# Performance work log

Hardware: AMD Instinct MI355X
Metric: run time of the kernel (lower is better)

The kernel has to match this reference:

```python
import jax, jax.numpy as jnp
import numpy as np

N_F = 256
D = 4 * N_F          # d_model after PixelUnshuffle(2)
D_INNER = 2 * D      # mamba expand=2
D_STATE = 16
DT_RANK = D // 16
N_LAYERS = 8
BATCH = 16
IMG = 32


def _pixel_unshuffle(x, r):
    b, c, h, w = x.shape
    x = x.reshape(b, c, h // r, r, w // r, r)
    return x.transpose(0, 1, 3, 5, 2, 4).reshape(b, c * r * r, h // r, w // r)


def _pixel_shuffle(x, r):
    b, c, h, w = x.shape
    co = c // (r * r)
    x = x.reshape(b, co, r, r, h, w)
    return x.transpose(0, 1, 4, 2, 5, 3).reshape(b, co, h * r, w * r)


def _layernorm(x, w, b):
    mu = jnp.mean(x, -1, keepdims=True)
    var = jnp.mean((x - mu) ** 2, -1, keepdims=True)
    return (x - mu) * jax.lax.rsqrt(var + 1e-5) * w + b


def _transpose_xy(a):
    b, l, c = a.shape
    s = int(np.sqrt(l))
    return a.reshape(b, s, s, c).transpose(0, 2, 1, 3).reshape(b, l, c)


def _mamba_mixer(u, W_in_i, conv_w_i, conv_b_i, W_x_i, W_dt_i, b_dt_i, A_log_i, D_skip_i, W_out_i):
    b, l, d = u.shape
    xz = jnp.einsum('bld,ed->ble', u, W_in_i)          # (B,L,2*d_inner)
    x, z = jnp.split(xz, 2, axis=-1)
    # causal depthwise conv over sequence, kernel 4, left-pad 3
    xt = jax.lax.conv_general_dilated(
        x.transpose(0, 2, 1), conv_w_i[:, None, :], (1,), [(3, 0)],
        feature_group_count=D_INNER, dimension_numbers=('NCH', 'OIH', 'NCH'))
    x = jax.nn.silu((xt + conv_b_i[None, :, None]).transpose(0, 2, 1))  # (B,L,d_inner)
    dbc = jnp.einsum('ble,fe->blf', x, W_x_i)          # (B,L,dt_rank+2*d_state)
    dt = jax.nn.softplus(jnp.einsum('blr,er->ble', dbc[..., :DT_RANK], W_dt_i) + b_dt_i)
    Bm = dbc[..., DT_RANK:DT_RANK + D_STATE]
    Cm = dbc[..., DT_RANK + D_STATE:]
    A = -jnp.exp(A_log_i)                              # (d_inner, d_state)

    def step(h, inp):
        dt_t, B_t, C_t, x_t = inp                      # (B,di),(B,ds),(B,ds),(B,di)
        h = jnp.exp(dt_t[..., None] * A) * h + (dt_t * x_t)[..., None] * B_t[:, None, :]
        return h, jnp.einsum('bds,bs->bd', h, C_t)

    h0 = jnp.zeros((b, D_INNER, D_STATE), dtype=u.dtype)
    _, ys = jax.lax.scan(step, h0, (dt.transpose(1, 0, 2), Bm.transpose(1, 0, 2),
                                    Cm.transpose(1, 0, 2), x.transpose(1, 0, 2)))
    y = ys.transpose(1, 0, 2) + x * D_skip_i
    y = y * jax.nn.silu(z)
    return jnp.einsum('ble,de->bld', y, W_out_i)


def setup_inputs() -> dict:
    key = jax.random.key(0)
    ks = jax.random.split(key, 20)
    s = 0.02
    inp = {
        'x': jax.random.normal(ks[0], (BATCH, 3, IMG, IMG), jnp.float32),
        'noise_level': jax.random.uniform(ks[1], (BATCH, 1, 1, 1), jnp.float32),
        'pe_w1': jax.random.normal(ks[2], (N_F, 4), jnp.float32) * s,
        'pe_b1': jnp.zeros((N_F,), jnp.float32),
        'pe_w2': jax.random.normal(ks[3], (N_F, N_F), jnp.float32) * s,
        'ln_w': jnp.ones((N_LAYERS, D), jnp.float32),
        'ln_b': jnp.zeros((N_LAYERS, D), jnp.float32),
        'W_in': jax.random.normal(ks[4], (N_LAYERS, 2 * D_INNER, D), jnp.float32) * s,
        'conv_w': jax.random.normal(ks[5], (N_LAYERS, D_INNER, 4), jnp.float32) * s,
        'conv_b': jnp.zeros((N_LAYERS, D_INNER), jnp.float32),
        'W_x': jax.random.normal(ks[6], (N_LAYERS, DT_RANK + 2 * D_STATE, D_INNER), jnp.float32) * s,
        'W_dt': jax.random.normal(ks[7], (N_LAYERS, D_INNER, DT_RANK), jnp.float32) * s,
        'b_dt': jax.random.normal(ks[8], (N_LAYERS, D_INNER), jnp.float32) * s,
        'A_log': jnp.broadcast_to(jnp.log(jnp.arange(1, D_STATE + 1, dtype=jnp.float32)),
                                  (N_LAYERS, D_INNER, D_STATE)),
        'D_skip': jnp.ones((N_LAYERS, D_INNER), jnp.float32),
        'W_out': jax.random.normal(ks[9], (N_LAYERS, D, D_INNER), jnp.float32) * s,
        'op_w1': jax.random.normal(ks[10], (4 * N_F, 12 * N_F), jnp.float32) * s,
        'op_b1': jnp.zeros((4 * N_F,), jnp.float32),
        'op_w2': jax.random.normal(ks[11], (3, N_F), jnp.float32) * s,
        'op_b2': jnp.zeros((3,), jnp.float32),
    }
    return inp


def reference(x, noise_level, pe_w1, pe_b1, pe_w2, ln_w, ln_b, W_in, conv_w, conv_b,
              W_x, W_dt, b_dt, A_log, D_skip, W_out, op_w1, op_b1, op_w2, op_b2):
    B, _, H, W = x.shape
    nl = jnp.broadcast_to(noise_level, (B, 1, H, W))
    h = jnp.concatenate([x, nl], axis=1)                       # (B,4,H,W)
    h = jax.nn.relu(jnp.einsum('bchw,oc->bohw', h, pe_w1) + pe_b1[None, :, None, None])
    h = jnp.einsum('bchw,oc->bohw', h, pe_w2)
    X = _pixel_unshuffle(h, 2)                                 # (B,4*n_f,H/2,W/2)
    Bc, C, Hh, Ww = X.shape
    y = X.reshape(Bc, C, Hh * Ww).transpose(0, 2, 1)           # (B,L,d_model)
    z = None
    for i in range(N_LAYERS):
        z = y if z is None else y + z                          # Block residual routing
        yn = _layernorm(z, ln_w[i], ln_b[i])
        y = _mamba_mixer(yn, W_in[i], conv_w[i], conv_b[i], W_x[i], W_dt[i], b_dt[i],
                         A_log[i], D_skip[i], W_out[i])
        y = _transpose_xy(y)
        z = _transpose_xy(z)
        if (i + 1) % 4 == 0:
            y = y[:, ::-1]
            z = z[:, ::-1]
    y2 = y.transpose(0, 2, 1).reshape(X.shape)
    z2 = z.transpose(0, 2, 1).reshape(X.shape)
    out = jnp.concatenate([X, y2, z2], axis=1)                 # (B,12*n_f,H/2,W/2)
    out = jax.nn.relu(jnp.einsum('bchw,oc->bohw', out, op_w1) + op_b1[None, :, None, None])
    out = _pixel_shuffle(out, 2)                               # (B,n_f,H,W)
    out = jnp.einsum('bchw,oc->bohw', out, op_w2) + op_b2[None, :, None, None]
    return out
```

## Files before the change

### kernel.cpp

```cpp
#include <hip/hip_runtime.h>

typedef unsigned short u16;
typedef __bf16 bf16x8 __attribute__((ext_vector_type(8)));
typedef float f32x4 __attribute__((ext_vector_type(4)));
typedef const __attribute__((address_space(1))) void* as1p;
typedef __attribute__((address_space(3))) void* as3p;

#define VMCNT4 asm volatile("s_waitcnt vmcnt(4)" ::: "memory")
#define LGKM0  asm volatile("s_waitcnt lgkmcnt(0)" ::: "memory")

__device__ __forceinline__ float bf2f(u16 h) { return __uint_as_float(((unsigned)h) << 16); }
__device__ __forceinline__ float ldf(const void* p, size_t i, int bf) {
    return bf ? bf2f(((const u16*)p)[i]) : ((const float*)p)[i];
}
__device__ __forceinline__ float4 ldf4(const void* p, size_t i, int bf) {
    if (bf) {
        const u16* q = (const u16*)p + i;
        ushort4 v = *(const ushort4*)q;
        return make_float4(bf2f(v.x), bf2f(v.y), bf2f(v.z), bf2f(v.w));
    }
    return *(const float4*)((const float*)p + i);
}
__device__ __forceinline__ u16 f2bf(float f) {
    unsigned u = __float_as_uint(f);
    unsigned r = (u + 0x7FFFu + ((u >> 16) & 1u)) >> 16;
    return (u16)r;
}
__device__ __forceinline__ float silu_f(float x) { return x * (1.f / (1.f + __expf(-x))); }

__device__ __forceinline__ int permL(int l, int rev) {
    if (rev) l = 255 - l;
    return ((l & 15) << 4) | (l >> 4);
}

__device__ __forceinline__ void gload_lds16(const void* g, void* l) {
    __builtin_amdgcn_global_load_lds((as1p)g, (as3p)l, 16, 0, 0);
}

__global__ void k_detect(const void* lnw, int* flag) {
    if (threadIdx.x == 0 && blockIdx.x == 0) {
        unsigned w = ((const unsigned*)lnw)[0];
        *flag = (w == 0x3F803F80u) ? 1 : 0;
    }
}

__global__ void k_cvt(const void* src, size_t soff, u16* __restrict__ dst, int n,
                      const int* __restrict__ flagp) {
    int bf = *flagp;
    int i4 = (blockIdx.x * 256 + threadIdx.x) * 4;
    if (i4 >= n) return;
    float4 v = ldf4(src, soff + i4, bf);
    *(ushort4*)(dst + i4) = make_ushort4(f2bf(v.x), f2bf(v.y), f2bf(v.z), f2bf(v.w));
}

__global__ void k_cvt_padx(const void* src, u16* __restrict__ dst,
                           const int* __restrict__ flagp) {
    int bf = *flagp;
    int i4 = (blockIdx.x * 256 + threadIdx.x) * 4;
    int row = i4 >> 11, col = i4 & 2047;
    int layer = row >> 7, lrow = row & 127;
    ushort4 o = make_ushort4(0, 0, 0, 0);
    if (lrow < 96) {
        float4 v = ldf4(src, (size_t)layer * 96 * 2048 + (size_t)lrow * 2048 + col, bf);
        o = make_ushort4(f2bf(v.x), f2bf(v.y), f2bf(v.z), f2bf(v.w));
    }
    *(ushort4*)(dst + i4) = o;
}

__global__ void k_head1(const void* x, const void* nl, const void* w1, const void* b1,
                        float* __restrict__ h1, const int* flagp) {
    int bf = *flagp;
    int idx = blockIdx.x * 256 + threadIdx.x;
    int o = idx & 255, p = (idx >> 8) & 1023, b = idx >> 18;
    float c0 = ldf(x, ((size_t)b * 3 + 0) * 1024 + p, bf);
    float c1 = ldf(x, ((size_t)b * 3 + 1) * 1024 + p, bf);
    float c2 = ldf(x, ((size_t)b * 3 + 2) * 1024 + p, bf);
    float c3 = ldf(nl, b, bf);
    float acc = ldf(w1, (size_t)o * 4 + 0, bf) * c0 + ldf(w1, (size_t)o * 4 + 1, bf) * c1 +
                ldf(w1, (size_t)o * 4 + 2, bf) * c2 + ldf(w1, (size_t)o * 4 + 3, bf) * c3 +
                ldf(b1, o, bf);
    h1[idx] = fmaxf(acc, 0.f);
}

template <int EPI>
__global__ __launch_bounds__(256) void k_gemm(
    const float* __restrict__ A, int lda,
    const void* __restrict__ W, size_t woff,
    const void* __restrict__ bias, size_t boff,
    float* __restrict__ C, int N, int K,
    const int* __restrict__ flagp, int perm) {
    int bf = *flagp;
    __shared__ float As[16][68];
    __shared__ float Ws[16][68];
    int t = threadIdx.x;
    int m0 = blockIdx.y * 64, n0 = blockIdx.x * 64;
    int lrow = t >> 2, lcol = (t & 3) << 2;
    int tx = t & 15, tyr = t >> 4;
    float acc[4][4] = {};
    for (int k0 = 0; k0 < K; k0 += 16) {
        float4 av = *(const float4*)(A + (size_t)(m0 + lrow) * lda + k0 + lcol);
        float4 wv = make_float4(0.f, 0.f, 0.f, 0.f);
        int nrow = n0 + lrow;
        if (nrow < N) wv = ldf4(W, woff + (size_t)nrow * K + k0 + lcol, bf);
        __syncthreads();
        As[lcol + 0][lrow] = av.x; As[lcol + 1][lrow] = av.y;
        As[lcol + 2][lrow] = av.z; As[lcol + 3][lrow] = av.w;
        Ws[lcol + 0][lrow] = wv.x; Ws[lcol + 1][lrow] = wv.y;
        Ws[lcol + 2][lrow] = wv.z; Ws[lcol + 3][lrow] = wv.w;
        __syncthreads();
#pragma unroll
        for (int k = 0; k < 16; ++k) {
            float4 a = *(const float4*)&As[k][tyr << 2];
            float4 bv = *(const float4*)&Ws[k][tx << 2];
            float aa[4] = {a.x, a.y, a.z, a.w};
            float bb[4] = {bv.x, bv.y, bv.z, bv.w};
#pragma unroll
            for (int i = 0; i < 4; ++i)
#pragma unroll
                for (int j = 0; j < 4; ++j) acc[i][j] += aa[i] * bb[j];
        }
    }
#pragma unroll
    for (int i = 0; i < 4; ++i) {
        int m = m0 + (tyr << 2) + i;
        int mo = m;
        if (perm >= 0) { int b = m >> 8, l = m & 255; mo = (b << 8) | permL(l, perm); }
#pragma unroll
        for (int j = 0; j < 4; ++j) {
            int n = n0 + (tx << 2) + j;
            if (n >= N) continue;
            float v = acc[i][j];
            if (EPI == 1) { v += ldf(bias, boff + n, bf); v = fmaxf(v, 0.f); }
            if (EPI == 2) { v += ldf(bias, boff + n, bf); v = (v > 20.f) ? v : log1pf(expf(v)); }
            C[(size_t)mo * N + n] = v;
        }
    }
}

__global__ __launch_bounds__(512, 2) void k_m256(
    const u16* __restrict__ A, int lda,
    const u16* __restrict__ W, int ldw,
    u16* __restrict__ C, int ldc, int nt) {
    __shared__ __align__(16) u16 Ab[2][2][128 * 64];
    __shared__ __align__(16) u16 Bb[2][2][128 * 64];
    int t = threadIdx.x;
    int w = t >> 6, lane = t & 63;
    int wm = w >> 2, wn = w & 3;
    int fr = lane & 15, q = lane >> 4;
    int flat = blockIdx.y * gridDim.x + blockIdx.x;
    int nwg = gridDim.x * gridDim.y, cpx = nwg >> 3;
    int tile = (flat & 7) * cpx + (flat >> 3);
    int bx = tile % gridDim.x, by = tile / gridDim.x;
    int m0 = by * 256, n0 = bx * 256;
    int sr = t >> 3, sslot = t & 7;

    auto stA = [&](int d, int kt, int h, int j) {
        int lr = j * 64 + sr;
        int gr = (lr >> 6) * 128 + h * 64 + (lr & 63);
        int col = kt * 64 + ((sslot ^ (lr & 7)) << 3);
        gload_lds16(A + (size_t)(m0 + gr) * lda + col, &Ab[d][h][lr * 64 + sslot * 8]);
    };
    auto stB = [&](int d, int kt, int h, int j) {
        int lr = j * 64 + sr;
        int gr = (lr >> 5) * 64 + h * 32 + (lr & 31);
        int col = kt * 64 + ((sslot ^ (lr & 7)) << 3);
        gload_lds16(W + (size_t)(n0 + gr) * ldw + col, &Bb[d][h][lr * 64 + sslot * 8]);
    };
    auto ldA = [&](int d, int mf, int kk) {
        int lr = wm * 64 + (mf & 3) * 16 + fr;
        int sl = (kk * 4 + q) ^ (lr & 7);
        return *(const bf16x8*)&Ab[d][mf >> 2][lr * 64 + sl * 8];
    };
    auto ldB = [&](int d, int nf, int kk) {
        int lr = wn * 32 + (nf & 1) * 16 + fr;
        int sl = (kk * 4 + q) ^ (lr & 7);
        return *(const bf16x8*)&Bb[d][nf >> 1][lr * 64 + sl * 8];
    };

    f32x4 acc[8][4] = {};
    bf16x8 av[4][2], bv0[2][2], bv1[2][2];

    stA(0, 0, 0, 0); stA(0, 0, 0, 1); stA(0, 0, 1, 0); stA(0, 0, 1, 1);
    stB(0, 0, 0, 0); stB(0, 0, 0, 1); stB(0, 0, 1, 0); stB(0, 0, 1, 1);
    asm volatile("s_waitcnt vmcnt(0)" ::: "memory");
    __builtin_amdgcn_s_barrier();

    for (int kt = 0; kt < nt; ++kt) {
        int d = kt & 1, nd = d ^ 1, nk = kt + 1;
        bool more = nk < nt;
        VMCNT4;
        __builtin_amdgcn_s_barrier();
        if (more) { stA(nd, nk, 0, 0); stA(nd, nk, 0, 1); }
#pragma unroll
        for (int m = 0; m < 4; ++m) { av[m][0] = ldA(d, m, 0); av[m][1] = ldA(d, m, 1); }
#pragma unroll
        for (int n = 0; n < 2; ++n) { bv0[n][0] = ldB(d, n, 0); bv0[n][1] = ldB(d, n, 1); }
        LGKM0; __builtin_amdgcn_sched_barrier(0);
        __builtin_amdgcn_s_setprio(1);
#pragma unroll
        for (int m = 0; m < 4; ++m)
#pragma unroll
            for (int n = 0; n < 2; ++n) {
                acc[m][n] = __builtin_amdgcn_mfma_f32_16x16x32_bf16(av[m][0], bv0[n][0], acc[m][n], 0, 0, 0);
                acc[m][n] = __builtin_amdgcn_mfma_f32_16x16x32_bf16(av[m][1], bv0[n][1], acc[m][n], 0, 0, 0);
            }
        __builtin_amdgcn_s_setprio(0);
        VMCNT4;
        __builtin_amdgcn_s_barrier();
        if (more) { stB(nd, nk, 0, 0); stB(nd, nk, 0, 1); }
#pragma unroll
        for (int n = 0; n < 2; ++n) { bv1[n][0] = ldB(d, n + 2, 0); bv1[n][1] = ldB(d, n + 2, 1); }
        LGKM0; __builtin_amdgcn_sched_barrier(0);
        __builtin_amdgcn_s_setprio(1);
#pragma unroll
        for (int m = 0; m < 4; ++m)
#pragma unroll
            for (int n = 0; n < 2; ++n) {
                acc[m][n + 2] = __builtin_amdgcn_mfma_f32_16x16x32_bf16(av[m][0], bv1[n][0], acc[m][n + 2], 0, 0, 0);
                acc[m][n + 2] = __builtin_amdgcn_mfma_f32_16x16x32_bf16(av[m][1], bv1[n][1], acc[m][n + 2], 0, 0, 0);
            }
        __builtin_amdgcn_s_setprio(0);
        VMCNT4;
        __builtin_amdgcn_s_barrier();
        if (more) { stB(nd, nk, 1, 0); stB(nd, nk, 1, 1); }
#pragma unroll
        for (int m = 0; m < 4; ++m) { av[m][0] = ldA(d, m + 4, 0); av[m][1] = ldA(d, m + 4, 1); }
        LGKM0; __builtin_amdgcn_sched_barrier(0);
        __builtin_amdgcn_s_setprio(1);
#pragma unroll
        for (int m = 0; m < 4; ++m)
#pragma unroll
            for (int n = 0; n < 2; ++n) {
                acc[m + 4][n] = __builtin_amdgcn_mfma_f32_16x16x32_bf16(av[m][0], bv0[n][0], acc[m + 4][n], 0, 0, 0);
                acc[m + 4][n] = __builtin_amdgcn_mfma_f32_16x16x32_bf16(av[m][1], bv0[n][1], acc[m + 4][n], 0, 0, 0);
            }
        __builtin_amdgcn_s_setprio(0);
        VMCNT4;
        __builtin_amdgcn_s_barrier();
        if (more) { stA(nd, nk, 1, 0); stA(nd, nk, 1, 1); }
        __builtin_amdgcn_s_setprio(1);
#pragma unroll
        for (int m = 0; m < 4; ++m)
#pragma unroll
            for (int n = 0; n < 2; ++n) {
                acc[m + 4][n + 2] = __builtin_amdgcn_mfma_f32_16x16x32_bf16(av[m][0], bv1[n][0], acc[m + 4][n + 2], 0, 0, 0);
                acc[m + 4][n + 2] = __builtin_amdgcn_mfma_f32_16x16x32_bf16(av[m][1], bv1[n][1], acc[m + 4][n + 2], 0, 0, 0);
            }
        __builtin_amdgcn_s_setprio(0);
    }
#pragma unroll
    for (int m = 0; m < 8; ++m) {
        int row = m0 + wm * 128 + m * 16 + q * 4;
#pragma unroll
        for (int rr = 0; rr < 4; ++rr)
#pragma unroll
            for (int n = 0; n < 4; ++n)
                C[(size_t)(row + rr) * ldc + n0 + wn * 64 + n * 16 + fr] = f2bf(acc[m][n][rr]);
    }
}

template <int EPI, int OUT16, int BN>
__global__ __launch_bounds__(256) void k_mgemm(
    const u16* __restrict__ A, int lda,
    const u16* __restrict__ W, int ldw,
    const void* __restrict__ bias, size_t boff,
    void* __restrict__ Cv, int ldc, int N,
    int ktPerZ, int perm, const int* __restrict__ flagp) {
    constexpr int NF = BN / 32;
    int bf = *flagp;
    __shared__ __align__(16) u16 As[128 * 32];
    __shared__ __align__(16) u16 Bs[BN * 32];
    int t = threadIdx.x;
    int gx = gridDim.x;
    int flat = blockIdx.y * gx + blockIdx.x;
    int nwg = gx * gridDim.y;
    if ((nwg & 7) == 0) {
        int cpx = nwg >> 3;
        flat = (flat & 7) * cpx + (flat >> 3);
    }
    int bx = flat % gx, by = flat / gx;
    int m0 = by * 128, n0 = bx * BN;
    int kt0 = blockIdx.z * ktPerZ;
    float* Cf = (float*)Cv + (size_t)blockIdx.z * (size_t)gridDim.y * 128 * ldc;
    u16* Ch = (u16*)Cv;
    int w = t >> 6, lane = t & 63;
    int wm = w >> 1, wn = w & 1;
    int fr = lane & 15, kb = (lane >> 4) * 8;
    int srow = lane >> 2, scol = (lane & 3) * 8;
    f32x4 acc[4][NF] = {};
    for (int kt = kt0; kt < kt0 + ktPerZ; ++kt) {
        int kc = kt * 32;
#pragma unroll
        for (int i = 0; i < 2; ++i) {
            int r = i * 64 + w * 16 + srow;
            gload_lds16(A + (size_t)(m0 + r) * lda + kc + scol, As + i * 2048 + w * 512);
        }
#pragma unroll
        for (int i = 0; i < BN / 64; ++i) {
            int r = i * 64 + w * 16 + srow;
            gload_lds16(W + (size_t)(n0 + r) * ldw + kc + scol, Bs + i * 2048 + w * 512);
        }
        __syncthreads();
        bf16x8 af[4], bv[NF];
#pragma unroll
        for (int m = 0; m < 4; ++m)
            af[m] = *(const bf16x8*)(As + (wm * 64 + m * 16 + fr) * 32 + kb);
#pragma unroll
        for (int n = 0; n < NF; ++n)
            bv[n] = *(const bf16x8*)(Bs + (wn * NF * 16 + n * 16 + fr) * 32 + kb);
#pragma unroll
        for (int m = 0; m < 4; ++m)
#pragma unroll
            for (int n = 0; n < NF; ++n)
                acc[m][n] = __builtin_amdgcn_mfma_f32_16x16x32_bf16(af[m], bv[n], acc[m][n], 0, 0, 0);
        __syncthreads();
    }
    int r0 = (lane >> 4) * 4;
#pragma unroll
    for (int m = 0; m < 4; ++m) {
        int rowb = m0 + wm * 64 + m * 16 + r0;
#pragma unroll
        for (int rr = 0; rr < 4; ++rr) {
            int row = rowb + rr;
            int mo = row;
            if (perm >= 0) { int bb = row >> 8, l = row & 255; mo = (bb << 8) | permL(l, perm); }
#pragma unroll
            for (int n = 0; n < NF; ++n) {
                int col = n0 + wn * NF * 16 + n * 16 + fr;
                if (col >= N) continue;
                float v = acc[m][n][rr];
                if (EPI == 1) { v += ldf(bias, boff + col, bf); v = fmaxf(v, 0.f); }
                if (EPI == 2) { v += ldf(bias, boff + col, bf); v = (v > 20.f) ? v : log1pf(expf(v)); }
                if (OUT16) Ch[(size_t)mo * ldc + col] = f2bf(v);
                else       Cf[(size_t)mo * ldc + col] = v;
            }
        }
    }
}

__global__ void k_xred(const float* __restrict__ part, float* __restrict__ dbc,
                       u16* __restrict__ dbc16) {
    int idx = blockIdx.x * 256 + threadIdx.x;
    int m = idx / 96, n = idx - m * 96;
    float s = 0.f;
#pragma unroll
    for (int z = 0; z < 8; ++z) s += part[(size_t)z * 4096 * 128 + (size_t)m * 128 + n];
    dbc[idx] = s;
    dbc16[idx] = f2bf(s);
}

__global__ void k_rearr(const float* __restrict__ h2, float* __restrict__ X) {
    int idx = blockIdx.x * 256 + threadIdx.x;
    int d = idx & 1023, l = (idx >> 10) & 255, b = idx >> 18;
    int o = d >> 2, r1 = (d >> 1) & 1, r2 = d & 1;
    int hh = l >> 4, ww = l & 15;
    int p = ((hh << 1) | r1) * 32 + ((ww << 1) | r2);
    X[idx] = h2[((size_t)b * 1024 + p) * 256 + o];
}

__global__ __launch_bounds__(256) void k_ln(
    const float* __restrict__ yin, const float* __restrict__ zold,
    float* __restrict__ znew, u16* __restrict__ yn16,
    const void* lnw, const void* lnb, size_t lno,
    const int* __restrict__ flagp, int prevPerm, int first) {
    int bf = *flagp;
    int m = blockIdx.x, b = m >> 8, l = m & 255;
    int t = threadIdx.x;
    float4 v = *(const float4*)(yin + (size_t)m * 1024 + (t << 2));
    if (!first) {
        int l2 = permL(l, prevPerm);
        float4 zv = *(const float4*)(zold + ((size_t)((b << 8) | l2)) * 1024 + (t << 2));
        v.x += zv.x; v.y += zv.y; v.z += zv.z; v.w += zv.w;
    }
    *(float4*)(znew + (size_t)m * 1024 + (t << 2)) = v;
    float s = v.x + v.y + v.z + v.w;
    float s2 = v.x * v.x + v.y * v.y + v.z * v.z + v.w * v.w;
#pragma unroll
    for (int o = 32; o > 0; o >>= 1) { s += __shfl_down(s, o, 64); s2 += __shfl_down(s2, o, 64); }
    __shared__ float red[8];
    __shared__ float mv[2];
    int wid = t >> 6;
    if ((t & 63) == 0) { red[wid] = s; red[4 + wid] = s2; }
    __syncthreads();
    if (t == 0) {
        float a = red[0] + red[1] + red[2] + red[3];
        float c = red[4] + red[5] + red[6] + red[7];
        float mu = a * (1.f / 1024.f);
        mv[0] = mu;
        mv[1] = rsqrtf(c * (1.f / 1024.f) - mu * mu + 1e-5f);
    }
    __syncthreads();
    float mu = mv[0], rs = mv[1];
    size_t wb = lno + (t << 2);
    float o0 = (v.x - mu) * rs * ldf(lnw, wb + 0, bf) + ldf(lnb, wb + 0, bf);
    float o1 = (v.y - mu) * rs * ldf(lnw, wb + 1, bf) + ldf(lnb, wb + 1, bf);
    float o2 = (v.z - mu) * rs * ldf(lnw, wb + 2, bf) + ldf(lnb, wb + 2, bf);
    float o3 = (v.w - mu) * rs * ldf(lnw, wb + 3, bf) + ldf(lnb, wb + 3, bf);
    *(ushort4*)(yn16 + (size_t)m * 1024 + (t << 2)) =
        make_ushort4(f2bf(o0), f2bf(o1), f2bf(o2), f2bf(o3));
}

__global__ void k_conv(const u16* __restrict__ xz16, const void* cw, size_t cwo,
                       const void* cb, size_t cbo,
                       u16* __restrict__ xc16, const int* __restrict__ flagp) {
    int bf = *flagp;
    int idx = blockIdx.x * 256 + threadIdx.x;
    int c = idx & 2047, l = (idx >> 11) & 255, b = idx >> 19;
    float w0 = ldf(cw, cwo + (size_t)c * 4 + 0, bf);
    float w1 = ldf(cw, cwo + (size_t)c * 4 + 1, bf);
    float w2 = ldf(cw, cwo + (size_t)c * 4 + 2, bf);
    float w3 = ldf(cw, cwo + (size_t)c * 4 + 3, bf);
    size_t base = ((size_t)b * 256) * 4096 + c;
    float acc = ldf(cb, cbo + c, bf);
    if (l >= 3) acc += w0 * bf2f(xz16[base + (size_t)(l - 3) * 4096]);
    if (l >= 2) acc += w1 * bf2f(xz16[base + (size_t)(l - 2) * 4096]);
    if (l >= 1) acc += w2 * bf2f(xz16[base + (size_t)(l - 1) * 4096]);
    acc += w3 * bf2f(xz16[base + (size_t)l * 4096]);
    xc16[idx] = f2bf(silu_f(acc));
}

__global__ __launch_bounds__(256) void k_scan_a(
    const float* __restrict__ dbc, const float* __restrict__ dt,
    const u16* __restrict__ xc16, const void* A_log, size_t ao,
    float* __restrict__ hsum, float* __restrict__ sumdt,
    const int* __restrict__ flagp) {
    int bf = *flagp;
    __shared__ float Bs[32][16];
    int t = threadIdx.x;
    int bid = blockIdx.x;
    int dg = bid & 7, ch = (bid >> 3) & 7, b = bid >> 6;
    int d = dg * 256 + t, l0 = ch * 32;
    if (t < 128) {
        int l = t >> 2, q = (t & 3) * 4;
        *(float4*)&Bs[l][q] = *(const float4*)(dbc + (size_t)(b * 256 + l0 + l) * 96 + 64 + q);
    }
    float aneg[16];
#pragma unroll
    for (int s = 0; s < 16; ++s) aneg[s] = -__expf(ldf(A_log, ao + (size_t)d * 16 + s, bf));
    float h[16];
#pragma unroll
    for (int s = 0; s < 16; ++s) h[s] = 0.f;
    float sd = 0.f;
    __syncthreads();
    const float* dtp = dt + (size_t)(b * 256 + l0) * 2048 + d;
    const u16* xp = xc16 + (size_t)(b * 256 + l0) * 2048 + d;
#pragma unroll
    for (int half = 0; half < 2; ++half) {
        float dtv[16], xv[16];
#pragma unroll
        for (int j = 0; j < 16; ++j) {
            dtv[j] = dtp[(size_t)(half * 16 + j) * 2048];
            xv[j] = bf2f(xp[(size_t)(half * 16 + j) * 2048]);
        }
#pragma unroll
        for (int j = 0; j < 16; ++j) {
            int l = half * 16 + j;
            float dx = dtv[j] * xv[j];
#pragma unroll
            for (int s = 0; s < 16; ++s) {
                float e = __expf(dtv[j] * aneg[s]);
                h[s] = e * h[s] + dx * Bs[l][s];
            }
            sd += dtv[j];
        }
    }
    size_t base = ((size_t)(b * 8 + ch) * 16) * 2048 + d;
#pragma unroll
    for (int s = 0; s < 16; ++s) hsum[base + (size_t)s * 2048] = h[s];
    sumdt[(size_t)(b * 8 + ch) * 2048 + d] = sd;
}

__global__ __launch_bounds__(256) void k_scan_c(
    const float* __restrict__ dbc, const float* __restrict__ dt,
    const u16* __restrict__ xc16, const u16* __restrict__ xz16,
    const float* __restrict__ hsum, const float* __restrict__ sumdt,
    const void* A_log, size_t ao,
    const void* Dsk, size_t doo, u16* __restrict__ ys16,
    const int* __restrict__ flagp) {
    int bf = *flagp;
    __shared__ float Bs[32][16];
    __shared__ float Cs[32][16];
    int t = threadIdx.x;
    int bid = blockIdx.x;
    int dg = bid & 7, ch = (bid >> 3) & 7, b = bid >> 6;
    int d = dg * 256 + t, l0 = ch * 32;
    if (t < 128) {
        int l = t >> 2, q = (t & 3) * 4;
        const float* row = dbc + (size_t)(b * 256 + l0 + l) * 96;
        *(float4*)&Bs[l][q] = *(const float4*)(row + 64 + q);
        *(float4*)&Cs[l][q] = *(const float4*)(row + 80 + q);
    }
    float aneg[16];
#pragma unroll
    for (int s = 0; s < 16; ++s) aneg[s] = -__expf(ldf(A_log, ao + (size_t)d * 16 + s, bf));
    float h[16];
#pragma unroll
    for (int s = 0; s < 16; ++s) h[s] = 0.f;
    for (int c = 0; c < ch; ++c) {
        float sd = sumdt[(size_t)(b * 8 + c) * 2048 + d];
        size_t hb = ((size_t)(b * 8 + c) * 16) * 2048 + d;
#pragma unroll
        for (int s = 0; s < 16; ++s)
            h[s] = __expf(aneg[s] * sd) * h[s] + hsum[hb + (size_t)s * 2048];
    }
    float Dv = ldf(Dsk, doo + d, bf);
    __syncthreads();
    const float* dtp = dt + (size_t)(b * 256 + l0) * 2048 + d;
    const u16* xp = xc16 + (size_t)(b * 256 + l0) * 2048 + d;
    const u16* zp = xz16 + (size_t)(b * 256 + l0) * 4096 + 2048 + d;
    u16* yp = ys16 + (size_t)(b * 256 + l0) * 2048 + d;
#pragma unroll
    for (int half = 0; half < 2; ++half) {
        float dtv[16], xv[16], zv[16];
#pragma unroll
        for (int j = 0; j < 16; ++j) {
            dtv[j] = dtp[(size_t)(half * 16 + j) * 2048];
            xv[j] = bf2f(xp[(size_t)(half * 16 + j) * 2048]);
            zv[j] = bf2f(zp[(size_t)(half * 16 + j) * 4096]);
        }
#pragma unroll
        for (int j = 0; j < 16; ++j) {
            int l = half * 16 + j;
            float dx = dtv[j] * xv[j];
            float acc = 0.f;
#pragma unroll
            for (int s = 0; s < 16; ++s) {
                float e = __expf(dtv[j] * aneg[s]);
                h[s] = e * h[s] + dx * Bs[l][s];
                acc += h[s] * Cs[l][s];
            }
            float v = (acc + xv[j] * Dv) * silu_f(zv[j]);
            yp[(size_t)l * 2048] = f2bf(v);
        }
    }
}

__global__ void k_concat(const float* __restrict__ X, const float* __restrict__ y,
                         const float* __restrict__ z, u16* __restrict__ cat16) {
    int idx = blockIdx.x * 256 + threadIdx.x;
    int c = idx % 3072;
    int m = idx / 3072;
    float v;
    if (c < 1024) v = X[(size_t)m * 1024 + c];
    else if (c < 2048) v = y[(size_t)m * 1024 + (c - 1024)];
    else {
        int b = m >> 8, l = m & 255;
        int l2 = permL(l, 1);
        v = z[((size_t)((b << 8) | l2)) * 1024 + (c - 2048)];
    }
    cat16[idx] = f2bf(v);
}

__global__ void k_final(const float* __restrict__ out1, const void* w2, const void* b2,
                        void* out, const int* __restrict__ flagp) {
    int bf = *flagp;
    int idx = blockIdx.x * 256 + threadIdx.x;
    int j = idx & 31, i = (idx >> 5) & 31, b = idx >> 10;
    int hh = i >> 1, r1 = i & 1, ww = j >> 1, r2 = j & 1;
    int l = (hh << 4) | ww, roff = (r1 << 1) | r2;
    const float* p = out1 + ((size_t)b * 256 + l) * 1024 + roff;
    float a0 = ldf(b2, 0, bf), a1 = ldf(b2, 1, bf), a2 = ldf(b2, 2, bf);
    for (int co = 0; co < 256; ++co) {
        float v = p[co << 2];
        a0 += v * ldf(w2, co, bf);
        a1 += v * ldf(w2, 256 + co, bf);
        a2 += v * ldf(w2, 512 + co, bf);
    }
    size_t o0 = ((size_t)b * 3) * 1024 + (i << 5) + j;
    if (bf) {
        u16* ob = (u16*)out;
        ob[o0] = f2bf(a0); ob[o0 + 1024] = f2bf(a1); ob[o0 + 2048] = f2bf(a2);
    } else {
        float* of = (float*)out;
        of[o0] = a0; of[o0 + 1024] = a1; of[o0 + 2048] = a2;
    }
}

extern "C" void kernel_launch(void* const* d_in, const int* in_sizes, int n_in,
                              void* d_out, int out_size, void* d_ws, size_t ws_size,
                              hipStream_t stream) {
    const void* I_x   = d_in[0];  const void* I_nl  = d_in[1];
    const void* I_pw1 = d_in[2];  const void* I_pb1 = d_in[3];
    const void* I_pw2 = d_in[4];  const void* I_lnw = d_in[5];
    const void* I_lnb = d_in[6];  const void* I_Win = d_in[7];
    const void* I_cw  = d_in[8];  const void* I_cb  = d_in[9];
    const void* I_Wx  = d_in[10]; const void* I_Wdt = d_in[11];
    const void* I_bdt = d_in[12]; const void* I_Alog = d_in[13];
    const void* I_Dsk = d_in[14]; const void* I_Wout = d_in[15];
    const void* I_ow1 = d_in[16]; const void* I_ob1 = d_in[17];
    const void* I_ow2 = d_in[18]; const void* I_ob2 = d_in[19];

    float* ws = (float*)d_ws;
    int* flag = (int*)d_ws;
    size_t off = 64;
    auto alloc = [&](size_t n) { float* p = ws + off; off += n; return p; };
    const size_t MD = 4096ull * 1024;
    float* Xs    = alloc(MD);
    float* y     = alloc(MD);
    float* za    = alloc(MD);
    float* zb    = alloc(MD);
    float* dbc   = alloc(4096ull * 96);
    float* dtb   = alloc(4096ull * 2048);
    float* hsum  = alloc(16ull * 8 * 16 * 2048);
    float* sumdt = alloc(16ull * 8 * 2048);
    u16* xz16  = (u16*)alloc(4096ull * 4096 / 2);
    u16* yn16  = (u16*)alloc(MD / 2);
    u16* ys16  = (u16*)alloc(MD);
    u16* xc16  = (u16*)alloc(MD);
    u16* dbc16 = (u16*)alloc(4096ull * 96 / 2);
    u16* wWin  = (u16*)alloc(8ull * 4096 * 1024 / 2);
    u16* wWx   = (u16*)alloc(8ull * 128 * 2048 / 2);
    u16* wWdt  = (u16*)alloc(8ull * 2048 * 64 / 2);
    u16* wWout = (u16*)alloc(8ull * 1024 * 2048 / 2);
    u16* wWop  = (u16*)alloc(1024ull * 3072 / 2);
    float* xpart = dtb + 4194304;
    float* h1 = dtb;
    float* out1 = y;
    u16* cat16 = yn16;
    float* h2 = y;
    float* zbufs[2] = {za, zb};

    k_detect<<<1, 64, 0, stream>>>(I_lnw, flag);

    k_cvt<<<32768, 256, 0, stream>>>(I_Win, 0, wWin, 8 * 4096 * 1024, flag);
    k_cvt_padx<<<2048, 256, 0, stream>>>(I_Wx, wWx, flag);
    k_cvt<<<1024, 256, 0, stream>>>(I_Wdt, 0, wWdt, 8 * 2048 * 64, flag);
    k_cvt<<<16384, 256, 0, stream>>>(I_Wout, 0, wWout, 8 * 1024 * 2048, flag);
    k_cvt<<<3072, 256, 0, stream>>>(I_ow1, 0, wWop, 1024 * 3072, flag);

    k_head1<<<16384, 256, 0, stream>>>(I_x, I_nl, I_pw1, I_pb1, h1, flag);
    k_gemm<0><<<dim3(4, 256), 256, 0, stream>>>(h1, 256, I_pw2, 0, nullptr, 0, h2, 256, 256, flag, -1);
    k_rearr<<<16384, 256, 0, stream>>>(h2, Xs);

    for (int i = 0; i < 8; ++i) {
        int rev = (i == 3 || i == 7) ? 1 : 0;
        int prevPerm = (i >= 1) ? ((i - 1 == 3) ? 1 : 0) : 0;
        const float* yin = (i == 0) ? Xs : y;
        float* znew = zbufs[i & 1];
        float* zold = zbufs[(i & 1) ^ 1];
        size_t ao = (size_t)i * 2048 * 16;
        k_ln<<<4096, 256, 0, stream>>>(yin, zold, znew, yn16, I_lnw, I_lnb,
                                       (size_t)i * 1024, flag, prevPerm, i == 0);
        k_m256<<<dim3(16, 16), 512, 0, stream>>>(
            yn16, 1024, wWin + (size_t)i * 4096 * 1024, 1024, xz16, 4096, 16);
        k_conv<<<32768, 256, 0, stream>>>(xz16, I_cw, (size_t)i * 2048 * 4, I_cb,
                                          (size_t)i * 2048, xc16, flag);
        k_mgemm<0, 0, 128><<<dim3(1, 32, 8), 256, 0, stream>>>(
            xc16, 2048, wWx + (size_t)i * 128 * 2048, 2048, nullptr, 0,
            xpart, 128, 128, 8, -1, flag);
        k_xred<<<1536, 256, 0, stream>>>(xpart, dbc, dbc16);
        k_mgemm<2, 0, 128><<<dim3(16, 32), 256, 0, stream>>>(
            dbc16, 96, wWdt + (size_t)i * 2048 * 64, 64, I_bdt, (size_t)i * 2048,
            dtb, 2048, 2048, 2, -1, flag);
        k_scan_a<<<1024, 256, 0, stream>>>(dbc, dtb, xc16, I_Alog, ao, hsum, sumdt, flag);
        k_scan_c<<<1024, 256, 0, stream>>>(dbc, dtb, xc16, xz16, hsum, sumdt, I_Alog, ao,
                                           I_Dsk, (size_t)i * 2048, ys16, flag);
        k_mgemm<0, 0, 64><<<dim3(16, 32), 256, 0, stream>>>(
            ys16, 2048, wWout + (size_t)i * 1024 * 2048, 2048, nullptr, 0,
            y, 1024, 1024, 64, rev, flag);
    }

    k_concat<<<49152, 256, 0, stream>>>(Xs, y, zbufs[1], cat16);
    k_mgemm<1, 0, 64><<<dim3(16, 32), 256, 0, stream>>>(
        cat16, 3072, wWop, 3072, I_ob1, 0, out1, 1024, 1024, 96, -1, flag);
    k_final<<<64, 256, 0, stream>>>(out1, I_ow2, I_ob2, d_out, flag);
}
```

Measured before the change: 2.628 ms.

## Route out-projection and head GEMMs through split-K 256x256 MFMA kernel with reduction

Adds a split-K mode with fp32 partial output to the 256x256 MFMA GEMM kernel. The per-layer W_out projection and the final 3072-wide head GEMM now use it with four K-splits, followed by a new reduction kernel that sums the partials, applies bias/ReLU and the sequence permutation. The goal is the higher MFMA efficiency of the big-tile kernel, which the old smaller-tile GEMM did not get. In exchange it writes and rereads four 16 MB fp32 partial buffers and adds an extra launch per GEMM.

```diff
diff --git a/kernel.cpp b/kernel.cpp
--- a/kernel.cpp
+++ b/kernel.cpp
@@ -137,10 +137,11 @@
     }
 }
 
+template <int OUT16>
 __global__ __launch_bounds__(512, 2) void k_m256(
     const u16* __restrict__ A, int lda,
     const u16* __restrict__ W, int ldw,
-    u16* __restrict__ C, int ldc, int nt) {
+    void* __restrict__ Cv, int ldc, int ktPerZ) {
     __shared__ __align__(16) u16 Ab[2][2][128 * 64];
     __shared__ __align__(16) u16 Bb[2][2][128 * 64];
     int t = threadIdx.x;
@@ -152,6 +153,7 @@
     int tile = (flat & 7) * cpx + (flat >> 3);
     int bx = tile % gridDim.x, by = tile / gridDim.x;
     int m0 = by * 256, n0 = bx * 256;
+    int kt0 = blockIdx.z * ktPerZ;
     int sr = t >> 3, sslot = t & 7;
 
     auto stA = [&](int d, int kt, int h, int j) {
@@ -180,14 +182,14 @@
     f32x4 acc[8][4] = {};
     bf16x8 av[4][2], bv0[2][2], bv1[2][2];
 
-    stA(0, 0, 0, 0); stA(0, 0, 0, 1); stA(0, 0, 1, 0); stA(0, 0, 1, 1);
-    stB(0, 0, 0, 0); stB(0, 0, 0, 1); stB(0, 0, 1, 0); stB(0, 0, 1, 1);
+    stA(0, kt0, 0, 0); stA(0, kt0, 0, 1); stA(0, kt0, 1, 0); stA(0, kt0, 1, 1);
+    stB(0, kt0, 0, 0); stB(0, kt0, 0, 1); stB(0, kt0, 1, 0); stB(0, kt0, 1, 1);
     asm volatile("s_waitcnt vmcnt(0)" ::: "memory");
     __builtin_amdgcn_s_barrier();
 
-    for (int kt = 0; kt < nt; ++kt) {
-        int d = kt & 1, nd = d ^ 1, nk = kt + 1;
-        bool more = nk < nt;
+    for (int kt = kt0; kt < kt0 + ktPerZ; ++kt) {
+        int d = (kt - kt0) & 1, nd = d ^ 1, nk = kt + 1;
+        bool more = nk < kt0 + ktPerZ;
         VMCNT4;
         __builtin_amdgcn_s_barrier();
         if (more) { stA(nd, nk, 0, 0); stA(nd, nk, 0, 1); }
@@ -248,14 +250,28 @@
             }
         __builtin_amdgcn_s_setprio(0);
     }
-#pragma unroll
-    for (int m = 0; m < 8; ++m) {
-        int row = m0 + wm * 128 + m * 16 + q * 4;
-#pragma unroll
-        for (int rr = 0; rr < 4; ++rr)
-#pragma unroll
-            for (int n = 0; n < 4; ++n)
-                C[(size_t)(row + rr) * ldc + n0 + wn * 64 + n * 16 + fr] = f2bf(acc[m][n][rr]);
+    if (OUT16) {
+        u16* Ch = (u16*)Cv;
+#pragma unroll
+        for (int m = 0; m < 8; ++m) {
+            int row = m0 + wm * 128 + m * 16 + q * 4;
+#pragma unroll
+            for (int rr = 0; rr < 4; ++rr)
+#pragma unroll
+                for (int n = 0; n < 4; ++n)
+                    Ch[(size_t)(row + rr) * ldc + n0 + wn * 64 + n * 16 + fr] = f2bf(acc[m][n][rr]);
+        }
+    } else {
+        float* Cf = (float*)Cv + (size_t)blockIdx.z * (size_t)gridDim.y * 256 * ldc;
+#pragma unroll
+        for (int m = 0; m < 8; ++m) {
+            int row = m0 + wm * 128 + m * 16 + q * 4;
+#pragma unroll
+            for (int rr = 0; rr < 4; ++rr)
+#pragma unroll
+                for (int n = 0; n < 4; ++n)
+                    Cf[(size_t)(row + rr) * ldc + n0 + wn * 64 + n * 16 + fr] = acc[m][n][rr];
+        }
     }
 }
 
@@ -336,6 +352,29 @@
             }
         }
     }
+}
+
+template <int EPI>
+__global__ void k_ored(const float* __restrict__ part, float* __restrict__ out,
+                       const void* __restrict__ bias,
+                       const int* __restrict__ flagp, int perm, int nz) {
+    int bf = *flagp;
+    int idx4 = (blockIdx.x * 256 + threadIdx.x) * 4;
+    int m = idx4 >> 10, n = idx4 & 1023;
+    float4 s = make_float4(0.f, 0.f, 0.f, 0.f);
+    for (int z = 0; z < nz; ++z) {
+        float4 p = *(const float4*)(part + (size_t)z * 4096 * 1024 + (size_t)m * 1024 + n);
+        s.x += p.x; s.y += p.y; s.z += p.z; s.w += p.w;
+    }
+    if (EPI == 1) {
+        s.x = fmaxf(s.x + ldf(bias, n + 0, bf), 0.f);
+        s.y = fmaxf(s.y + ldf(bias, n + 1, bf), 0.f);
+        s.z = fmaxf(s.z + ldf(bias, n + 2, bf), 0.f);
+        s.w = fmaxf(s.w + ldf(bias, n + 3, bf), 0.f);
+    }
+    int mo = m;
+    if (perm >= 0) { int b = m >> 8, l = m & 255; mo = (b << 8) | permL(l, perm); }
+    *(float4*)(out + (size_t)mo * 1024 + n) = s;
 }
 
 __global__ void k_xred(const float* __restrict__ part, float* __restrict__ dbc,
@@ -603,6 +642,7 @@
     float* dtb   = alloc(4096ull * 2048);
     float* hsum  = alloc(16ull * 8 * 16 * 2048);
     float* sumdt = alloc(16ull * 8 * 2048);
+    float* opart = alloc(4ull * 4096 * 1024);
     u16* xz16  = (u16*)alloc(4096ull * 4096 / 2);
     u16* yn16  = (u16*)alloc(MD / 2);
     u16* ys16  = (u16*)alloc(MD);
@@ -641,7 +681,7 @@
         size_t ao = (size_t)i * 2048 * 16;
         k_ln<<<4096, 256, 0, stream>>>(yin, zold, znew, yn16, I_lnw, I_lnb,
                                        (size_t)i * 1024, flag, prevPerm, i == 0);
-        k_m256<<<dim3(16, 16), 512, 0, stream>>>(
+        k_m256<1><<<dim3(16, 16), 512, 0, stream>>>(
             yn16, 1024, wWin + (size_t)i * 4096 * 1024, 1024, xz16, 4096, 16);
         k_conv<<<32768, 256, 0, stream>>>(xz16, I_cw, (size_t)i * 2048 * 4, I_cb,
                                           (size_t)i * 2048, xc16, flag);
@@ -655,13 +695,14 @@
         k_scan_a<<<1024, 256, 0, stream>>>(dbc, dtb, xc16, I_Alog, ao, hsum, sumdt, flag);
         k_scan_c<<<1024, 256, 0, stream>>>(dbc, dtb, xc16, xz16, hsum, sumdt, I_Alog, ao,
                                            I_Dsk, (size_t)i * 2048, ys16, flag);
-        k_mgemm<0, 0, 64><<<dim3(16, 32), 256, 0, stream>>>(
-            ys16, 2048, wWout + (size_t)i * 1024 * 2048, 2048, nullptr, 0,
-            y, 1024, 1024, 64, rev, flag);
+        k_m256<0><<<dim3(4, 16, 4), 512, 0, stream>>>(
+            ys16, 2048, wWout + (size_t)i * 1024 * 2048, 2048, opart, 1024, 8);
+        k_ored<0><<<4096, 256, 0, stream>>>(opart, y, nullptr, flag, rev, 4);
     }
 
     k_concat<<<49152, 256, 0, stream>>>(Xs, y, zbufs[1], cat16);
-    k_mgemm<1, 0, 64><<<dim3(16, 32), 256, 0, stream>>>(
-        cat16, 3072, wWop, 3072, I_ob1, 0, out1, 1024, 1024, 96, -1, flag);
+    k_m256<0><<<dim3(4, 16, 4), 512, 0, stream>>>(
+        cat16, 3072, wWop, 3072, opart, 1024, 12);
+    k_ored<1><<<4096, 256, 0, stream>>>(opart, out1, I_ob1, flag, -1, 4);
     k_final<<<64, 256, 0, stream>>>(out1, I_ow2, I_ob2, d_out, flag);
 }
```

After: 2.588 ms. Within noise of the previous version (-1.5%).
